# Performance work log

Hardware: AMD Instinct MI355X
Metric: run time of the kernel (lower is better)

## Reference

```python
import jax, jax.numpy as jnp
import numpy as np

B, NCH, NPX = 64, 32, 20000
BETA = 1.0 / np.tanh(1.0)  # ReTanh(alpha=1.0) scale


def setup_inputs() -> dict:
    key = jax.random.key(0)
    ks = jax.random.split(key, 8)
    Xr = jax.random.normal(ks[0], (B, NCH, NCH), jnp.float32)
    Xi = jax.random.normal(ks[1], (B, NCH, NCH), jnp.float32)
    X = (Xr + 1j * Xi).astype(jnp.complex64)
    # Hermitian PSD covariance so eigh + sqrt(eigvals) is well-posed
    S = jnp.einsum('bij,bkj->bik', X, jnp.conj(X)) / NCH
    tau = 1e-5 * jax.random.normal(ks[2], (NPX,), jnp.float32)
    D_real = 0.1 * jax.random.normal(ks[3], (NCH, NPX), jnp.float32)
    D_imag = 0.1 * jax.random.normal(ks[4], (NCH, NPX), jnp.float32)
    A_real = jax.random.normal(ks[5], (NCH, NPX), jnp.float32) / np.sqrt(NCH)
    A_imag = jax.random.normal(ks[6], (NCH, NPX), jnp.float32) / np.sqrt(NCH)
    return {
        'S_real': jnp.real(S)[:, None],  # (B,1,NCH,NCH), squeezed in forward
        'S_imag': jnp.imag(S)[:, None],
        'tau': tau,
        'D_real': D_real,
        'D_imag': D_imag,
        'A_real': A_real,
        'A_imag': A_imag,
    }


def reference(S_real, S_imag, tau, D_real, D_imag, A_real, A_imag):
    S = (S_real + 1j * S_imag).astype(jnp.complex64)[:, 0]  # squeeze(1) -> (B,NCH,NCH)
    D = (D_real + 1j * D_imag).astype(jnp.complex64)        # (NCH,NPX)
    A = (A_real + 1j * A_imag).astype(jnp.complex64)        # (NCH,NPX)

    Ds, Vs = jnp.linalg.eigh(S)                     # Ds: (B,NCH) real, Vs: (B,NCH,NCH)
    Ds = jnp.where(Ds > 0, Ds, jnp.zeros_like(Ds))  # clamp negative eigenvalues
    Vs = Vs * jnp.sqrt(Ds)[:, None, :].astype(Vs.dtype)  # scale eigenvector columns

    # latent_x = || D^H @ Vs ||^2 over eigenvector index -> (B,NPX)
    lat = jnp.einsum('cp,bcd->bpd', jnp.conj(D), Vs)     # (B,NPX,NCH)
    latent = jnp.sum(jnp.real(lat) ** 2 + jnp.imag(lat) ** 2, axis=2)
    latent = latent - tau
    latent = jnp.maximum(jnp.asarray(1e-6, latent.dtype), BETA * jnp.tanh(latent))  # ReTanh

    # out = A @ diag(latent) @ A^H without materializing (NPX,NPX) diagonal
    lam = latent.astype(jnp.complex64)
    out = jnp.einsum('cp,bp,dp->bcd', A, lam, jnp.conj(A))  # (B,NCH,NCH)
    return out, latent
```

## Files before the change

kernel.cpp:

```cpp
#include <hip/hip_runtime.h>
#include <math.h>

#define B_SZ 64
#define NCH 32
#define NPX 20000
#define BETA_C 1.3130352854993312f
#define NCHUNKS 625
#define OB 25
#define CPB 25

typedef _Float16 f16;
typedef __attribute__((ext_vector_type(2)))  f16   h2;
typedef __attribute__((ext_vector_type(4)))  f16   h4;
typedef __attribute__((ext_vector_type(8)))  f16   h8;
typedef __attribute__((ext_vector_type(16))) float f32x16;
typedef __attribute__((ext_vector_type(8)))  short short8;

__device__ __forceinline__ h2 pk_f16(float a, float b) {
    return __builtin_bit_cast(h2, __builtin_amdgcn_cvt_pkrtz(a, b));
}

__global__ __launch_bounds__(256) void prep_kernel(
    const float* __restrict__ A_real, const float* __restrict__ A_imag,
    const float* __restrict__ D_real, const float* __restrict__ D_imag,
    f16* __restrict__ Ah_r, f16* __restrict__ Ah_i,
    f16* __restrict__ Dth_r, f16* __restrict__ Dth_i)
{
    __shared__ float s[NCH][257];
    const int t = threadIdx.x;
    const int bx = blockIdx.x;
    if (bx < 1250) {
        const int f = (bx * 256 + t) * 4;
        const int N = NCH * NPX;
        const float* src; f16* dst; int off;
        if (f < N) { src = A_real; dst = Ah_r; off = f; }
        else       { src = A_imag; dst = Ah_i; off = f - N; }
        const float4 v = *(const float4*)(src + off);
        h4 o = { (f16)v.x, (f16)v.y, (f16)v.z, (f16)v.w };
        *(h4*)(dst + off) = o;
        return;
    }
    const int p = (bx - 1250) * 256 + t;
    for (int plane = 0; plane < 2; ++plane) {
        const float* src = plane ? D_imag : D_real;
        f16* dst = plane ? Dth_i : Dth_r;
        __syncthreads();
        for (int c = 0; c < NCH; ++c)
            if (p < NPX) s[c][t] = src[(size_t)c * NPX + p];
        __syncthreads();
        if (p < NPX) {
#pragma unroll
            for (int q = 0; q < 4; ++q) {
                h8 wv;
#pragma unroll
                for (int e = 0; e < 8; ++e) wv[e] = (f16)s[q * 8 + e][t];
                *(h8*)(dst + (size_t)p * NCH + q * 8) = wv;
            }
        }
    }
}

__global__ __launch_bounds__(256) void latent_mfma(
    const float* __restrict__ S_real, const float* __restrict__ S_imag,
    const float* __restrict__ tau,
    const f16* __restrict__ Dth_r, const f16* __restrict__ Dth_i,
    float* __restrict__ lam_out)
{
    const int b   = blockIdx.y;
    const int t   = threadIdx.x;
    const int w   = t >> 6;
    const int l   = t & 63;
    const int l31 = l & 31;
    const int kh  = l >> 5;

    const float* srp = S_real + (size_t)b * 1024 + l31 * 32 + 8 * kh;
    const float* sip = S_imag + (size_t)b * 1024 + l31 * 32 + 8 * kh;
    h8 Sr0, Sr1, Si0, Si1, nSi0, nSi1;
#pragma unroll
    for (int j = 0; j < 8; ++j) {
        Sr0[j] = (f16)srp[j];      Sr1[j] = (f16)srp[16 + j];
        const float v0 = sip[j], v1 = sip[16 + j];
        Si0[j]  = (f16)v0;   Si1[j]  = (f16)v1;
        nSi0[j] = (f16)(-v0); nSi1[j] = (f16)(-v1);
    }

    const int base = blockIdx.x * CPB;
    const int end  = min(NCHUNKS, base + CPB);
    for (int ci = base + w; ci < end; ci += 4) {
        const int p0 = ci * 32;
        const int p  = p0 + l31;

        const f16* dbr = Dth_r + (size_t)p * 32 + 8 * kh;
        const f16* dbi = Dth_i + (size_t)p * 32 + 8 * kh;
        const h8 Dr0 = *(const h8*)(dbr);
        const h8 Dr1 = *(const h8*)(dbr + 16);
        const h8 Di0 = *(const h8*)(dbi);
        const h8 Di1 = *(const h8*)(dbi + 16);

        f32x16 Tr = {}, Ti = {};
        Tr = __builtin_amdgcn_mfma_f32_32x32x16_f16(Sr0,  Dr0, Tr, 0, 0, 0);
        Ti = __builtin_amdgcn_mfma_f32_32x32x16_f16(Sr0,  Di0, Ti, 0, 0, 0);
        Tr = __builtin_amdgcn_mfma_f32_32x32x16_f16(Sr1,  Dr1, Tr, 0, 0, 0);
        Ti = __builtin_amdgcn_mfma_f32_32x32x16_f16(Sr1,  Di1, Ti, 0, 0, 0);
        Tr = __builtin_amdgcn_mfma_f32_32x32x16_f16(nSi0, Di0, Tr, 0, 0, 0);
        Ti = __builtin_amdgcn_mfma_f32_32x32x16_f16(Si0,  Dr0, Ti, 0, 0, 0);
        Tr = __builtin_amdgcn_mfma_f32_32x32x16_f16(nSi1, Di1, Tr, 0, 0, 0);
        Ti = __builtin_amdgcn_mfma_f32_32x32x16_f16(Si1,  Dr1, Ti, 0, 0, 0);

        const f16* ddr = Dth_r + (size_t)p * 32 + 4 * kh;
        const f16* ddi = Dth_i + (size_t)p * 32 + 4 * kh;
        float part0 = 0.f, part1 = 0.f;
#pragma unroll
        for (int g = 0; g < 4; ++g) {
            const h4 dr = *(const h4*)(ddr + g * 8);
            const h4 di = *(const h4*)(ddi + g * 8);
#pragma unroll
            for (int r = 0; r < 4; ++r) {
                part0 = fmaf((float)dr[r], Tr[4 * g + r], part0);
                part1 = fmaf((float)di[r], Ti[4 * g + r], part1);
            }
        }
        float part = part0 + part1;
        part += __shfl_xor(part, 32, 64);

        const float lat = part - tau[p];
        const float lc  = fminf(fmaxf(lat, -15.f), 15.f);
        const float e   = __expf(2.f * lc);
        const float th  = __fdividef(e - 1.f, e + 1.f);
        const float lam = fmaxf(1e-6f, BETA_C * th);
        if (l < 32) lam_out[(size_t)b * NPX + p] = lam;
    }
}

__global__ __launch_bounds__(256) void outer_mfma(
    const f16* __restrict__ Ah_r, const f16* __restrict__ Ah_i,
    const float* __restrict__ lam_in, float* __restrict__ part)
{
    __shared__ float red[4][64][17];
    const int b   = blockIdx.y;
    const int t   = threadIdx.x;
    const int w   = t >> 6;
    const int l   = t & 63;
    const int row = l & 31;
    const int kh  = l >> 5;

    f32x16 accRe = {}, accIm = {};

    const int base = blockIdx.x * CPB;
    const int end  = min(NCHUNKS, base + CPB);
    for (int ci = base + w; ci < end; ci += 4) {
        const int p0 = ci * 32;
        const int pk = p0 + 8 * kh;

        const f16* ar_p = Ah_r + (size_t)row * NPX + pk;
        const f16* ai_p = Ah_i + (size_t)row * NPX + pk;
        const h8 ar0 = *(const h8*)(ar_p);
        const h8 ar1 = *(const h8*)(ar_p + 16);
        const h8 ai0 = *(const h8*)(ai_p);
        const h8 ai1 = *(const h8*)(ai_p + 16);

        const float* lp = lam_in + (size_t)b * NPX + pk;
        const float4 la = *(const float4*)(lp);
        const float4 lb = *(const float4*)(lp + 4);
        const float4 lc = *(const float4*)(lp + 16);
        const float4 ld = *(const float4*)(lp + 20);
        const h2 q0 = pk_f16(la.x, la.y);
        const h2 q1 = pk_f16(la.z, la.w);
        const h2 q2 = pk_f16(lb.x, lb.y);
        const h2 q3 = pk_f16(lb.z, lb.w);
        const h2 q4 = pk_f16(lc.x, lc.y);
        const h2 q5 = pk_f16(lc.z, lc.w);
        const h2 q6 = pk_f16(ld.x, ld.y);
        const h2 q7 = pk_f16(ld.z, ld.w);
        const h8 lam0 = {q0[0], q0[1], q1[0], q1[1], q2[0], q2[1], q3[0], q3[1]};
        const h8 lam1 = {q4[0], q4[1], q5[0], q5[1], q6[0], q6[1], q7[0], q7[1]};

        const h8 vr0 = ar0 * lam0;
        const h8 vi0 = ai0 * lam0;
        const h8 vr1 = ar1 * lam1;
        const h8 vi1 = ai1 * lam1;
        const h8 nvr0 = __builtin_bit_cast(h8, __builtin_bit_cast(short8, vr0) ^ (short)0x8000);
        const h8 nvr1 = __builtin_bit_cast(h8, __builtin_bit_cast(short8, vr1) ^ (short)0x8000);

        accRe = __builtin_amdgcn_mfma_f32_32x32x16_f16(vr0,  ar0, accRe, 0, 0, 0);
        accIm = __builtin_amdgcn_mfma_f32_32x32x16_f16(vi0,  ar0, accIm, 0, 0, 0);
        accRe = __builtin_amdgcn_mfma_f32_32x32x16_f16(vi0,  ai0, accRe, 0, 0, 0);
        accIm = __builtin_amdgcn_mfma_f32_32x32x16_f16(nvr0, ai0, accIm, 0, 0, 0);
        accRe = __builtin_amdgcn_mfma_f32_32x32x16_f16(vr1,  ar1, accRe, 0, 0, 0);
        accIm = __builtin_amdgcn_mfma_f32_32x32x16_f16(vi1,  ar1, accIm, 0, 0, 0);
        accRe = __builtin_amdgcn_mfma_f32_32x32x16_f16(vi1,  ai1, accRe, 0, 0, 0);
        accIm = __builtin_amdgcn_mfma_f32_32x32x16_f16(nvr1, ai1, accIm, 0, 0, 0);
    }

    float* pb = part + ((size_t)b * OB + blockIdx.x) * 2048;
#pragma unroll
    for (int r = 0; r < 16; ++r) red[w][l][r] = accRe[r];
    __syncthreads();
#pragma unroll
    for (int q = 0; q < 4; ++q) {
        const int idx = t + 256 * q;
        const int ll = idx >> 4, rr = idx & 15;
        const float s = red[0][ll][rr] + red[1][ll][rr] + red[2][ll][rr] + red[3][ll][rr];
        const int col  = ll & 31;
        const int orow = (rr & 3) + 8 * (rr >> 2) + 4 * (ll >> 5);
        pb[orow * 32 + col] = s;
    }
    __syncthreads();
#pragma unroll
    for (int r = 0; r < 16; ++r) red[w][l][r] = accIm[r];
    __syncthreads();
#pragma unroll
    for (int q = 0; q < 4; ++q) {
        const int idx = t + 256 * q;
        const int ll = idx >> 4, rr = idx & 15;
        const float s = red[0][ll][rr] + red[1][ll][rr] + red[2][ll][rr] + red[3][ll][rr];
        const int col  = ll & 31;
        const int orow = (rr & 3) + 8 * (rr >> 2) + 4 * (ll >> 5);
        pb[1024 + orow * 32 + col] = s;
    }
}

__global__ __launch_bounds__(256) void reduce_kernel(
    const float* __restrict__ part,
    float* __restrict__ out_re, float* __restrict__ out_im)
{
    const int b = blockIdx.x;
    const int t = threadIdx.x;
#pragma unroll
    for (int q = 0; q < 4; ++q) {
        const int slot = q * 256 + t;
        float sr = 0.f, si = 0.f;
        for (int k = 0; k < OB; ++k) {
            const float* pb = part + ((size_t)b * OB + k) * 2048;
            sr += pb[slot];
            si += pb[1024 + slot];
        }
        out_re[(size_t)b * 1024 + slot] = sr;
        if (out_im) out_im[(size_t)b * 1024 + slot] = si;
    }
}

extern "C" void kernel_launch(void* const* d_in, const int* in_sizes, int n_in,
                              void* d_out, int out_size, void* d_ws, size_t ws_size,
                              hipStream_t stream) {
    const float* S_real = (const float*)d_in[0];
    const float* S_imag = (const float*)d_in[1];
    const float* tau    = (const float*)d_in[2];
    const float* D_real = (const float*)d_in[3];
    const float* D_imag = (const float*)d_in[4];
    const float* A_real = (const float*)d_in[5];
    const float* A_imag = (const float*)d_in[6];

    f16* Ah_r  = (f16*)d_ws;
    f16* Ah_i  = Ah_r + (size_t)NCH * NPX;
    f16* Dth_r = Ah_i + (size_t)NCH * NPX;
    f16* Dth_i = Dth_r + (size_t)NCH * NPX;
    float* part = (float*)(Dth_i + (size_t)NCH * NPX);

    const size_t LAT = (size_t)B_SZ * NPX;
    const size_t RE  = (size_t)B_SZ * NCH * NCH;
    const size_t lam_off = (size_t)out_size - LAT;
    float* out_re = (float*)d_out;
    float* lam    = out_re + lam_off;
    float* out_im = (lam_off >= 2 * RE) ? out_re + RE : nullptr;

    prep_kernel<<<dim3(1250 + 79), 256, 0, stream>>>(
        A_real, A_imag, D_real, D_imag, Ah_r, Ah_i, Dth_r, Dth_i);

    latent_mfma<<<dim3(OB, B_SZ), 256, 0, stream>>>(
        S_real, S_imag, tau, Dth_r, Dth_i, lam);

    outer_mfma<<<dim3(OB, B_SZ), 256, 0, stream>>>(
        Ah_r, Ah_i, lam, part);

    reduce_kernel<<<dim3(B_SZ), 256, 0, stream>>>(part, out_re, out_im);
}
```

Before: 145.9 us.

## Pre-pack A and D into MFMA fragment order for contiguous per-lane loads

New measurement: 127.9 us. 12.3% less time.

```diff
diff --git a/kernel.cpp b/kernel.cpp
--- a/kernel.cpp
+++ b/kernel.cpp
@@ -23,38 +23,44 @@
 __global__ __launch_bounds__(256) void prep_kernel(
     const float* __restrict__ A_real, const float* __restrict__ A_imag,
     const float* __restrict__ D_real, const float* __restrict__ D_imag,
-    f16* __restrict__ Ah_r, f16* __restrict__ Ah_i,
-    f16* __restrict__ Dth_r, f16* __restrict__ Dth_i)
+    f16* __restrict__ AfR, f16* __restrict__ AfI,
+    f16* __restrict__ DfR, f16* __restrict__ DfI)
 {
     __shared__ float s[NCH][257];
-    const int t = threadIdx.x;
+    const int t  = threadIdx.x;
     const int bx = blockIdx.x;
-    if (bx < 1250) {
-        const int f = (bx * 256 + t) * 4;
-        const int N = NCH * NPX;
-        const float* src; f16* dst; int off;
-        if (f < N) { src = A_real; dst = Ah_r; off = f; }
-        else       { src = A_imag; dst = Ah_i; off = f - N; }
-        const float4 v = *(const float4*)(src + off);
-        h4 o = { (f16)v.x, (f16)v.y, (f16)v.z, (f16)v.w };
-        *(h4*)(dst + off) = o;
-        return;
-    }
-    const int p = (bx - 1250) * 256 + t;
-    for (int plane = 0; plane < 2; ++plane) {
-        const float* src = plane ? D_imag : D_real;
-        f16* dst = plane ? Dth_i : Dth_r;
+    const int p  = bx * 256 + t;
+    const int lc = t >> 5;
+    const int ci = bx * 8 + lc;
+    const int c31 = t & 31;
+
+    for (int plane = 0; plane < 4; ++plane) {
+        const float* src = (plane == 0) ? A_real : (plane == 1) ? A_imag
+                         : (plane == 2) ? D_real : D_imag;
         __syncthreads();
         for (int c = 0; c < NCH; ++c)
             if (p < NPX) s[c][t] = src[(size_t)c * NPX + p];
         __syncthreads();
-        if (p < NPX) {
-#pragma unroll
-            for (int q = 0; q < 4; ++q) {
+        if (ci >= NCHUNKS) continue;
+        if (plane < 2) {
+            f16* dst = (plane == 0) ? AfR : AfI;
+#pragma unroll
+            for (int pb = 0; pb < 4; ++pb) {
                 h8 wv;
 #pragma unroll
-                for (int e = 0; e < 8; ++e) wv[e] = (f16)s[q * 8 + e][t];
-                *(h8*)(dst + (size_t)p * NCH + q * 8) = wv;
+                for (int e = 0; e < 8; ++e)
+                    wv[e] = (f16)s[c31][lc * 32 + pb * 8 + e];
+                *(h8*)(dst + (((size_t)ci * 4 + pb) * 32 + c31) * 8) = wv;
+            }
+        } else {
+            f16* dst = (plane == 2) ? DfR : DfI;
+#pragma unroll
+            for (int g = 0; g < 4; ++g) {
+                h8 wv;
+#pragma unroll
+                for (int e = 0; e < 8; ++e)
+                    wv[e] = (f16)s[g * 8 + e][t];
+                *(h8*)(dst + (((size_t)ci * 4 + g) * 32 + c31) * 8) = wv;
             }
         }
     }
@@ -63,9 +69,10 @@
 __global__ __launch_bounds__(256) void latent_mfma(
     const float* __restrict__ S_real, const float* __restrict__ S_imag,
     const float* __restrict__ tau,
-    const f16* __restrict__ Dth_r, const f16* __restrict__ Dth_i,
+    const f16* __restrict__ DfR, const f16* __restrict__ DfI,
     float* __restrict__ lam_out)
 {
+    __shared__ float sre[NCH * 33], sim[NCH * 33];
     const int b   = blockIdx.y;
     const int t   = threadIdx.x;
     const int w   = t >> 6;
@@ -73,13 +80,20 @@
     const int l31 = l & 31;
     const int kh  = l >> 5;
 
-    const float* srp = S_real + (size_t)b * 1024 + l31 * 32 + 8 * kh;
-    const float* sip = S_imag + (size_t)b * 1024 + l31 * 32 + 8 * kh;
+    for (int i = t; i < NCH * NCH; i += 256) {
+        const int c = i >> 5, k = i & 31;
+        sre[c * 33 + k] = S_real[(size_t)b * 1024 + i];
+        sim[c * 33 + k] = S_imag[(size_t)b * 1024 + i];
+    }
+    __syncthreads();
+
+    const int i0 = l31 * 33 + 8 * kh;
     h8 Sr0, Sr1, Si0, Si1, nSi0, nSi1;
 #pragma unroll
     for (int j = 0; j < 8; ++j) {
-        Sr0[j] = (f16)srp[j];      Sr1[j] = (f16)srp[16 + j];
-        const float v0 = sip[j], v1 = sip[16 + j];
+        Sr0[j] = (f16)sre[i0 + j];
+        Sr1[j] = (f16)sre[i0 + 16 + j];
+        const float v0 = sim[i0 + j], v1 = sim[i0 + 16 + j];
         Si0[j]  = (f16)v0;   Si1[j]  = (f16)v1;
         nSi0[j] = (f16)(-v0); nSi1[j] = (f16)(-v1);
     }
@@ -87,15 +101,11 @@
     const int base = blockIdx.x * CPB;
     const int end  = min(NCHUNKS, base + CPB);
     for (int ci = base + w; ci < end; ci += 4) {
-        const int p0 = ci * 32;
-        const int p  = p0 + l31;
-
-        const f16* dbr = Dth_r + (size_t)p * 32 + 8 * kh;
-        const f16* dbi = Dth_i + (size_t)p * 32 + 8 * kh;
-        const h8 Dr0 = *(const h8*)(dbr);
-        const h8 Dr1 = *(const h8*)(dbr + 16);
-        const h8 Di0 = *(const h8*)(dbi);
-        const h8 Di1 = *(const h8*)(dbi + 16);
+        const size_t cb = (size_t)ci * 1024;
+        const h8 Dr0 = *(const h8*)(DfR + cb + l * 8);
+        const h8 Dr1 = *(const h8*)(DfR + cb + 512 + l * 8);
+        const h8 Di0 = *(const h8*)(DfI + cb + l * 8);
+        const h8 Di1 = *(const h8*)(DfI + cb + 512 + l * 8);
 
         f32x16 Tr = {}, Ti = {};
         Tr = __builtin_amdgcn_mfma_f32_32x32x16_f16(Sr0,  Dr0, Tr, 0, 0, 0);
@@ -107,13 +117,13 @@
         Tr = __builtin_amdgcn_mfma_f32_32x32x16_f16(nSi1, Di1, Tr, 0, 0, 0);
         Ti = __builtin_amdgcn_mfma_f32_32x32x16_f16(Si1,  Dr1, Ti, 0, 0, 0);
 
-        const f16* ddr = Dth_r + (size_t)p * 32 + 4 * kh;
-        const f16* ddi = Dth_i + (size_t)p * 32 + 4 * kh;
+        const f16* ddr = DfR + cb + l31 * 8 + 4 * kh;
+        const f16* ddi = DfI + cb + l31 * 8 + 4 * kh;
         float part0 = 0.f, part1 = 0.f;
 #pragma unroll
         for (int g = 0; g < 4; ++g) {
-            const h4 dr = *(const h4*)(ddr + g * 8);
-            const h4 di = *(const h4*)(ddi + g * 8);
+            const h4 dr = *(const h4*)(ddr + g * 256);
+            const h4 di = *(const h4*)(ddi + g * 256);
 #pragma unroll
             for (int r = 0; r < 4; ++r) {
                 part0 = fmaf((float)dr[r], Tr[4 * g + r], part0);
@@ -123,6 +133,7 @@
         float part = part0 + part1;
         part += __shfl_xor(part, 32, 64);
 
+        const int p = ci * 32 + l31;
         const float lat = part - tau[p];
         const float lc  = fminf(fmaxf(lat, -15.f), 15.f);
         const float e   = __expf(2.f * lc);
@@ -133,7 +144,7 @@
 }
 
 __global__ __launch_bounds__(256) void outer_mfma(
-    const f16* __restrict__ Ah_r, const f16* __restrict__ Ah_i,
+    const f16* __restrict__ AfR, const f16* __restrict__ AfI,
     const float* __restrict__ lam_in, float* __restrict__ part)
 {
     __shared__ float red[4][64][17];
@@ -141,7 +152,6 @@
     const int t   = threadIdx.x;
     const int w   = t >> 6;
     const int l   = t & 63;
-    const int row = l & 31;
     const int kh  = l >> 5;
 
     f32x16 accRe = {}, accIm = {};
@@ -149,16 +159,13 @@
     const int base = blockIdx.x * CPB;
     const int end  = min(NCHUNKS, base + CPB);
     for (int ci = base + w; ci < end; ci += 4) {
-        const int p0 = ci * 32;
-        const int pk = p0 + 8 * kh;
-
-        const f16* ar_p = Ah_r + (size_t)row * NPX + pk;
-        const f16* ai_p = Ah_i + (size_t)row * NPX + pk;
-        const h8 ar0 = *(const h8*)(ar_p);
-        const h8 ar1 = *(const h8*)(ar_p + 16);
-        const h8 ai0 = *(const h8*)(ai_p);
-        const h8 ai1 = *(const h8*)(ai_p + 16);
-
+        const size_t cb = (size_t)ci * 1024;
+        const h8 ar0 = *(const h8*)(AfR + cb + l * 8);
+        const h8 ar1 = *(const h8*)(AfR + cb + 512 + l * 8);
+        const h8 ai0 = *(const h8*)(AfI + cb + l * 8);
+        const h8 ai1 = *(const h8*)(AfI + cb + 512 + l * 8);
+
+        const int pk = ci * 32 + 8 * kh;
         const float* lp = lam_in + (size_t)b * NPX + pk;
         const float4 la = *(const float4*)(lp);
         const float4 lb = *(const float4*)(lp + 4);
@@ -251,11 +258,11 @@
     const float* A_real = (const float*)d_in[5];
     const float* A_imag = (const float*)d_in[6];
 
-    f16* Ah_r  = (f16*)d_ws;
-    f16* Ah_i  = Ah_r + (size_t)NCH * NPX;
-    f16* Dth_r = Ah_i + (size_t)NCH * NPX;
-    f16* Dth_i = Dth_r + (size_t)NCH * NPX;
-    float* part = (float*)(Dth_i + (size_t)NCH * NPX);
+    f16* AfR = (f16*)d_ws;
+    f16* AfI = AfR + (size_t)NCH * NPX;
+    f16* DfR = AfI + (size_t)NCH * NPX;
+    f16* DfI = DfR + (size_t)NCH * NPX;
+    float* part = (float*)(DfI + (size_t)NCH * NPX);
 
     const size_t LAT = (size_t)B_SZ * NPX;
     const size_t RE  = (size_t)B_SZ * NCH * NCH;
@@ -264,14 +271,14 @@
     float* lam    = out_re + lam_off;
     float* out_im = (lam_off >= 2 * RE) ? out_re + RE : nullptr;
 
-    prep_kernel<<<dim3(1250 + 79), 256, 0, stream>>>(
-        A_real, A_imag, D_real, D_imag, Ah_r, Ah_i, Dth_r, Dth_i);
+    prep_kernel<<<dim3(79), 256, 0, stream>>>(
+        A_real, A_imag, D_real, D_imag, AfR, AfI, DfR, DfI);
 
     latent_mfma<<<dim3(OB, B_SZ), 256, 0, stream>>>(
-        S_real, S_imag, tau, Dth_r, Dth_i, lam);
+        S_real, S_imag, tau, DfR, DfI, lam);
 
     outer_mfma<<<dim3(OB, B_SZ), 256, 0, stream>>>(
-        Ah_r, Ah_i, lam, part);
+        AfR, AfI, lam, part);
 
     reduce_kernel<<<dim3(B_SZ), 256, 0, stream>>>(part, out_re, out_im);
 }
```
